# Kernel tuning notes

Measured on AMD Instinct MI355X. Metric: run time of the kernel, lower is better.

The kernel has to match this reference:

```python
import jax, jax.numpy as jnp
import numpy as np

IN_FEATURES, OUT_FEATURES, KERNEL_DIMS = 1024, 128, 8
BATCH = 256


def setup_inputs() -> dict:
    key = jax.random.key(0)
    kx, kT = jax.random.split(key)
    x = jax.random.normal(kx, (BATCH, IN_FEATURES), dtype=jnp.float32)
    T = jax.random.normal(kT, (IN_FEATURES, OUT_FEATURES, KERNEL_DIMS), dtype=jnp.float32)
    return {"x": x, "T": T}


def reference(x, T):
    B = x.shape[0]
    in_f, out_f, kd = T.shape
    # M: (B, out_features, kernel_dims)
    M = (x @ T.reshape(in_f, out_f * kd)).reshape(B, out_f, kd)
    # pairwise L1 distance over kernel dims: (B, B, out_features)
    diffs = jnp.abs(M[None, :, :, :] - M[:, None, :, :]).sum(axis=3)
    # similarity features: sum over other samples, subtract self-term (exp(0)=1)
    c = jnp.exp(-diffs).sum(axis=1) - 1.0  # (B, out_features)
    return jnp.concatenate([x, c], axis=1)
```

## Files before the change

kernel.cpp:

```cpp
#include <hip/hip_runtime.h>
#include <stdint.h>

#define BATCH 256
#define INF   1024
#define OUTF  128
#define KD    8
#define NN    1024
#define OROW  1152

#define TSLP  1040
#define MLS   12
#define CHSH  16384
#define NBUF  4

typedef __attribute__((ext_vector_type(8))) short short8;
typedef __attribute__((ext_vector_type(4))) float f32x4;

__device__ __forceinline__ unsigned short f2bf(float f) {
    union { float f; uint32_t u; } v; v.f = f;
    uint32_t r = v.u + 0x7FFFu + ((v.u >> 16) & 1u);
    return (unsigned short)(r >> 16);
}

__global__ __launch_bounds__(256) void prep_kernel(
    const float* __restrict__ x, const float* __restrict__ T,
    float* __restrict__ out, unsigned short* __restrict__ xbf,
    unsigned short* __restrict__ Tt)
{
    __shared__ unsigned short lds[64 * 65];
    int bid = blockIdx.x;
    int t = threadIdx.x;
    if (bid < 256) {
        int i0 = (bid >> 4) << 6;
        int n0 = (bid & 15) << 6;
        int tx = t & 63, ty = t >> 6;
        for (int r = ty; r < 64; r += 4) {
            float v = T[(size_t)(i0 + r) * NN + n0 + tx];
            lds[tx * 65 + r] = f2bf(v);
        }
        __syncthreads();
        #pragma unroll
        for (int p = 0; p < 8; ++p) {
            int q = p * 512 + t * 2;
            int n = q >> 6, i = q & 63;
            uint32_t u = (uint32_t)lds[n * 65 + i] | ((uint32_t)lds[n * 65 + i + 1] << 16);
            *(uint32_t*)(Tt + (size_t)(n0 + n) * INF + i0 + i) = u;
        }
    } else {
        int bx = bid - 256;
        #pragma unroll
        for (int p = 0; p < 4; ++p) {
            int a = bx * 4 + p;
            int j = t * 4;
            float4 v = *(const float4*)(x + (size_t)a * INF + j);
            *(float4*)(out + (size_t)a * OROW + j) = v;
            uint2 u;
            u.x = (uint32_t)f2bf(v.x) | ((uint32_t)f2bf(v.y) << 16);
            u.y = (uint32_t)f2bf(v.z) | ((uint32_t)f2bf(v.w) << 16);
            *(uint2*)(xbf + (size_t)a * INF + j) = u;
        }
    }
}

__device__ __forceinline__ void stage_xb(
    const unsigned short* __restrict__ xbf, unsigned short* lbuf,
    int c, int wave, int lane)
{
    const int rin = lane >> 3;
    const int seg = lane & 7;
    #pragma unroll
    for (int p = 0; p < 4; ++p) {
        const int i = wave * 4 + p;
        const unsigned short* src = xbf + (size_t)(i * 8 + rin) * INF
                                        + c * 64 + ((seg ^ rin) << 3);
        unsigned short* dst = lbuf + i * 512;
        __builtin_amdgcn_global_load_lds(
            (const __attribute__((address_space(1))) unsigned int*)src,
            (__attribute__((address_space(3))) unsigned int*)dst, 16, 0, 0);
    }
}

#define GEMM_STEP(c, VM) do {                                                 \
    const uint32_t bb = xlsBase + (uint32_t)(((c) & 3) << 15);                \
    const uint32_t tb = tslBase + (uint32_t)((c) << 7);                       \
    short8 A00, A01, A10, A11, B0, B1;                                        \
    asm volatile(                                                             \
        "s_waitcnt vmcnt(" #VM ")\n\t"                                        \
        "ds_read_b128 %0, %6\n\t"                                             \
        "ds_read_b128 %1, %7\n\t"                                             \
        "ds_read_b128 %2, %8\n\t"                                             \
        "ds_read_b128 %3, %9\n\t"                                             \
        "ds_read_b128 %4, %10\n\t"                                            \
        "ds_read_b128 %5, %11\n\t"                                            \
        "s_waitcnt lgkmcnt(0)"                                                \
        : "=v"(A00), "=v"(A01), "=v"(A10), "=v"(A11), "=v"(B0), "=v"(B1)      \
        : "v"(bb + oA00), "v"(bb + oA01), "v"(bb + oA10), "v"(bb + oA11),     \
          "v"(tb + oB0), "v"(tb + oB1)                                        \
        : "memory");                                                          \
    acc0 = __builtin_amdgcn_mfma_f32_16x16x32_bf16(A00, B0, acc0, 0, 0, 0);   \
    acc0 = __builtin_amdgcn_mfma_f32_16x16x32_bf16(A01, B1, acc0, 0, 0, 0);   \
    acc1 = __builtin_amdgcn_mfma_f32_16x16x32_bf16(A10, B0, acc1, 0, 0, 0);   \
    acc1 = __builtin_amdgcn_mfma_f32_16x16x32_bf16(A11, B1, acc1, 0, 0, 0);   \
} while (0)

__global__ __launch_bounds__(512, 1) void fused_kernel(
    const unsigned short* __restrict__ xbf, const unsigned short* __restrict__ Tt,
    float* __restrict__ out)
{
    __shared__ __align__(16) unsigned short xls[NBUF * CHSH];
    __shared__ __align__(16) union {
        unsigned short Tsl[KD * TSLP];
        float red[512];
    } u;
    __shared__ __align__(16) float Mloc[256 * MLS];

    const int o = blockIdx.x >> 1;
    const int half = blockIdx.x & 1;
    const int t = threadIdx.x;
    const int wave = t >> 6, lane = t & 63;

    #pragma unroll
    for (int p = 0; p < 2; ++p) {
        const unsigned short* src = Tt + (size_t)(o * 8 + wave) * INF + p * 512 + lane * 8;
        unsigned short* dst = u.Tsl + wave * TSLP + p * 512;
        __builtin_amdgcn_global_load_lds(
            (const __attribute__((address_space(1))) unsigned int*)src,
            (__attribute__((address_space(3))) unsigned int*)dst, 16, 0, 0);
    }
    stage_xb(xbf, xls + 0 * CHSH, 0, wave, lane);
    stage_xb(xbf, xls + 1 * CHSH, 1, wave, lane);
    stage_xb(xbf, xls + 2 * CHSH, 2, wave, lane);
    __syncthreads();

    const int rc = lane & 15, quad = lane >> 4, r7 = rc & 7;
    const int abase = wave * 32;
    f32x4 acc0 = {0.f, 0.f, 0.f, 0.f}, acc1 = {0.f, 0.f, 0.f, 0.f};

    const uint32_t xlsBase = (uint32_t)(uintptr_t)(&xls[0]);
    const uint32_t tslBase = (uint32_t)(uintptr_t)(&u.Tsl[0]);
    const uint32_t rowA = (uint32_t)((abase + rc) * 128);
    const uint32_t oA00 = rowA + (uint32_t)(((0 * 4 + quad) ^ r7) << 4);
    const uint32_t oA01 = rowA + (uint32_t)(((1 * 4 + quad) ^ r7) << 4);
    const uint32_t oA10 = oA00 + 2048, oA11 = oA01 + 2048;
    const uint32_t oB0 = (uint32_t)(r7 * 2080 + quad * 16);
    const uint32_t oB1 = oB0 + 64;

    for (int c = 0; c < 13; ++c) {
        stage_xb(xbf, xls + ((c + 3) & 3) * CHSH, c + 3, wave, lane);
        GEMM_STEP(c, 12);
    }
    GEMM_STEP(13, 8);
    GEMM_STEP(14, 4);
    GEMM_STEP(15, 0);

    if (rc < 8) {
        #pragma unroll
        for (int r = 0; r < 4; ++r) {
            Mloc[(abase + quad * 4 + r) * MLS + rc]      = acc0[r];
            Mloc[(abase + 16 + quad * 4 + r) * MLS + rc] = acc1[r];
        }
    }
    __syncthreads();

    const int ar = t & 127;
    const int bq = t >> 7;
    const int a = half * 128 + ar;
    f32x4 m0 = *(const f32x4*)(Mloc + a * MLS);
    f32x4 m1 = *(const f32x4*)(Mloc + a * MLS + 4);
    float ssum = 0.f;
    #pragma unroll 4
    for (int j = 0; j < 64; ++j) {
        const float* qp = Mloc + (bq * 64 + j) * MLS;
        f32x4 q0 = *(const f32x4*)(qp);
        f32x4 q1 = *(const f32x4*)(qp + 4);
        float d = fabsf(m0[0] - q0[0]) + fabsf(m0[1] - q0[1])
                + fabsf(m0[2] - q0[2]) + fabsf(m0[3] - q0[3])
                + fabsf(m1[0] - q1[0]) + fabsf(m1[1] - q1[1])
                + fabsf(m1[2] - q1[2]) + fabsf(m1[3] - q1[3]);
        ssum += __expf(-d);
    }
    u.red[t] = ssum;
    __syncthreads();
    if (t < 128) {
        float s = u.red[t] + u.red[t + 128] + u.red[t + 256] + u.red[t + 384];
        out[(size_t)(half * 128 + t) * OROW + INF + o] = s - 1.0f;
    }
}

extern "C" void kernel_launch(void* const* d_in, const int* in_sizes, int n_in,
                              void* d_out, int out_size, void* d_ws, size_t ws_size,
                              hipStream_t stream) {
    const float* x = (const float*)d_in[0];
    const float* T = (const float*)d_in[1];
    float* out = (float*)d_out;
    unsigned short* xbf = (unsigned short*)d_ws;
    unsigned short* Tt  = (unsigned short*)((char*)d_ws + 524288);

    prep_kernel<<<320, 256, 0, stream>>>(x, T, out, xbf, Tt);
    fused_kernel<<<256, 512, 0, stream>>>(xbf, Tt, out);
}
```

Baseline: 70.82 us.

## Switch GEMM operands from bf16 to fp8 MFMA with deeper LDS pipeline

Converts x and T to fp8 (e4m3) in the prep kernel instead of bf16 and uses the fp8 16x16x32 MFMA with 64-bit LDS reads. This halves workspace traffic and LDS footprint per chunk, and the freed space is used for an 8-deep staging pipeline with 7 chunks prefetched. The cost is a large precision drop: fp8 has about a 3-bit mantissa, and the values of M feed exp(-L1 distance) across 8 dims summed over 1024 inputs. That risks exceeding tolerance.

Measured after the change: 72.79 us. 1.03x slower.

```diff
diff --git a/kernel.cpp b/kernel.cpp
--- a/kernel.cpp
+++ b/kernel.cpp
@@ -8,26 +8,19 @@
 #define NN    1024
 #define OROW  1152
 
-#define TSLP  1040
 #define MLS   12
-#define CHSH  16384
-#define NBUF  4
+#define CHB   16384
+#define NBUF  8
+#define TP8   1056
 
-typedef __attribute__((ext_vector_type(8))) short short8;
 typedef __attribute__((ext_vector_type(4))) float f32x4;
-
-__device__ __forceinline__ unsigned short f2bf(float f) {
-    union { float f; uint32_t u; } v; v.f = f;
-    uint32_t r = v.u + 0x7FFFu + ((v.u >> 16) & 1u);
-    return (unsigned short)(r >> 16);
-}
 
 __global__ __launch_bounds__(256) void prep_kernel(
     const float* __restrict__ x, const float* __restrict__ T,
-    float* __restrict__ out, unsigned short* __restrict__ xbf,
-    unsigned short* __restrict__ Tt)
+    float* __restrict__ out, unsigned char* __restrict__ x8,
+    unsigned char* __restrict__ Tt8)
 {
-    __shared__ unsigned short lds[64 * 65];
+    __shared__ unsigned char lds8[64 * 68];
     int bid = blockIdx.x;
     int t = threadIdx.x;
     if (bid < 256) {
@@ -36,15 +29,16 @@
         int tx = t & 63, ty = t >> 6;
         for (int r = ty; r < 64; r += 4) {
             float v = T[(size_t)(i0 + r) * NN + n0 + tx];
-            lds[tx * 65 + r] = f2bf(v);
+            lds8[tx * 68 + r] =
+                (unsigned char)(__builtin_amdgcn_cvt_pk_fp8_f32(v, v, 0, false) & 0xff);
         }
         __syncthreads();
         #pragma unroll
-        for (int p = 0; p < 8; ++p) {
-            int q = p * 512 + t * 2;
+        for (int p = 0; p < 4; ++p) {
+            int q = p * 1024 + t * 4;
             int n = q >> 6, i = q & 63;
-            uint32_t u = (uint32_t)lds[n * 65 + i] | ((uint32_t)lds[n * 65 + i + 1] << 16);
-            *(uint32_t*)(Tt + (size_t)(n0 + n) * INF + i0 + i) = u;
+            uint32_t w = *(const uint32_t*)(lds8 + n * 68 + i);
+            *(uint32_t*)(Tt8 + (size_t)(n0 + n) * INF + i0 + i) = w;
         }
     } else {
         int bx = bid - 256;
@@ -54,26 +48,25 @@
             int j = t * 4;
             float4 v = *(const float4*)(x + (size_t)a * INF + j);
             *(float4*)(out + (size_t)a * OROW + j) = v;
-            uint2 u;
-            u.x = (uint32_t)f2bf(v.x) | ((uint32_t)f2bf(v.y) << 16);
-            u.y = (uint32_t)f2bf(v.z) | ((uint32_t)f2bf(v.w) << 16);
-            *(uint2*)(xbf + (size_t)a * INF + j) = u;
+            uint32_t w = (uint32_t)__builtin_amdgcn_cvt_pk_fp8_f32(v.x, v.y, 0, false);
+            w = (uint32_t)__builtin_amdgcn_cvt_pk_fp8_f32(v.z, v.w, (int)w, true);
+            *(uint32_t*)(x8 + (size_t)a * INF + j) = w;
         }
     }
 }
 
-__device__ __forceinline__ void stage_xb(
-    const unsigned short* __restrict__ xbf, unsigned short* lbuf,
+__device__ __forceinline__ void stage_x8(
+    const unsigned char* __restrict__ x8, unsigned char* lbuf,
     int c, int wave, int lane)
 {
-    const int rin = lane >> 3;
-    const int seg = lane & 7;
+    const int r16 = lane >> 2;
+    const int slot = lane & 3;
     #pragma unroll
-    for (int p = 0; p < 4; ++p) {
-        const int i = wave * 4 + p;
-        const unsigned short* src = xbf + (size_t)(i * 8 + rin) * INF
-                                        + c * 64 + ((seg ^ rin) << 3);
-        unsigned short* dst = lbuf + i * 512;
+    for (int p = 0; p < 2; ++p) {
+        const int i = wave * 2 + p;
+        const unsigned char* src = x8 + (size_t)(i * 16 + r16) * INF
+                                       + c * 64 + ((slot ^ (r16 & 3)) << 4);
+        unsigned char* dst = lbuf + i * 1024;
         __builtin_amdgcn_global_load_lds(
             (const __attribute__((address_space(1))) unsigned int*)src,
             (__attribute__((address_space(3))) unsigned int*)dst, 16, 0, 0);
@@ -81,35 +74,35 @@
 }
 
 #define GEMM_STEP(c, VM) do {                                                 \
-    const uint32_t bb = xlsBase + (uint32_t)(((c) & 3) << 15);                \
-    const uint32_t tb = tslBase + (uint32_t)((c) << 7);                       \
-    short8 A00, A01, A10, A11, B0, B1;                                        \
+    const uint32_t bb = xlsBase + (uint32_t)(((c) & 7) * CHB);                \
+    const uint32_t tb = tslBase + oB + (uint32_t)((c) << 6);                  \
+    long long A00, A01, A10, A11, B0, B1;                                     \
     asm volatile(                                                             \
         "s_waitcnt vmcnt(" #VM ")\n\t"                                        \
-        "ds_read_b128 %0, %6\n\t"                                             \
-        "ds_read_b128 %1, %7\n\t"                                             \
-        "ds_read_b128 %2, %8\n\t"                                             \
-        "ds_read_b128 %3, %9\n\t"                                             \
-        "ds_read_b128 %4, %10\n\t"                                            \
-        "ds_read_b128 %5, %11\n\t"                                            \
+        "ds_read_b64 %0, %6\n\t"                                              \
+        "ds_read_b64 %1, %7\n\t"                                              \
+        "ds_read_b64 %2, %8\n\t"                                              \
+        "ds_read_b64 %3, %9\n\t"                                              \
+        "ds_read_b64 %4, %10\n\t"                                             \
+        "ds_read_b64 %5, %11\n\t"                                             \
         "s_waitcnt lgkmcnt(0)"                                                \
         : "=v"(A00), "=v"(A01), "=v"(A10), "=v"(A11), "=v"(B0), "=v"(B1)      \
-        : "v"(bb + oA00), "v"(bb + oA01), "v"(bb + oA10), "v"(bb + oA11),     \
-          "v"(tb + oB0), "v"(tb + oB1)                                        \
+        : "v"(bb + aA00), "v"(bb + aA01), "v"(bb + aA00 + 1024),              \
+          "v"(bb + aA01 + 1024), "v"(tb), "v"(tb + 32)                        \
         : "memory");                                                          \
-    acc0 = __builtin_amdgcn_mfma_f32_16x16x32_bf16(A00, B0, acc0, 0, 0, 0);   \
-    acc0 = __builtin_amdgcn_mfma_f32_16x16x32_bf16(A01, B1, acc0, 0, 0, 0);   \
-    acc1 = __builtin_amdgcn_mfma_f32_16x16x32_bf16(A10, B0, acc1, 0, 0, 0);   \
-    acc1 = __builtin_amdgcn_mfma_f32_16x16x32_bf16(A11, B1, acc1, 0, 0, 0);   \
+    acc0 = __builtin_amdgcn_mfma_f32_16x16x32_fp8_fp8(A00, B0, acc0, 0, 0, 0);\
+    acc0 = __builtin_amdgcn_mfma_f32_16x16x32_fp8_fp8(A01, B1, acc0, 0, 0, 0);\
+    acc1 = __builtin_amdgcn_mfma_f32_16x16x32_fp8_fp8(A10, B0, acc1, 0, 0, 0);\
+    acc1 = __builtin_amdgcn_mfma_f32_16x16x32_fp8_fp8(A11, B1, acc1, 0, 0, 0);\
 } while (0)
 
 __global__ __launch_bounds__(512, 1) void fused_kernel(
-    const unsigned short* __restrict__ xbf, const unsigned short* __restrict__ Tt,
+    const unsigned char* __restrict__ x8, const unsigned char* __restrict__ Tt8,
     float* __restrict__ out)
 {
-    __shared__ __align__(16) unsigned short xls[NBUF * CHSH];
+    __shared__ __align__(16) unsigned char xls[NBUF * CHB];
     __shared__ __align__(16) union {
-        unsigned short Tsl[KD * TSLP];
+        unsigned char Tsl[8 * TP8];
         float red[512];
     } u;
     __shared__ __align__(16) float Mloc[256 * MLS];
@@ -119,38 +112,41 @@
     const int t = threadIdx.x;
     const int wave = t >> 6, lane = t & 63;
 
-    #pragma unroll
-    for (int p = 0; p < 2; ++p) {
-        const unsigned short* src = Tt + (size_t)(o * 8 + wave) * INF + p * 512 + lane * 8;
-        unsigned short* dst = u.Tsl + wave * TSLP + p * 512;
+    {
+        const unsigned char* src = Tt8 + (size_t)(o * 8 + wave) * INF + lane * 16;
+        unsigned char* dst = u.Tsl + wave * TP8;
         __builtin_amdgcn_global_load_lds(
             (const __attribute__((address_space(1))) unsigned int*)src,
             (__attribute__((address_space(3))) unsigned int*)dst, 16, 0, 0);
     }
-    stage_xb(xbf, xls + 0 * CHSH, 0, wave, lane);
-    stage_xb(xbf, xls + 1 * CHSH, 1, wave, lane);
-    stage_xb(xbf, xls + 2 * CHSH, 2, wave, lane);
+    #pragma unroll
+    for (int c = 0; c < 7; ++c)
+        stage_x8(x8, xls + c * CHB, c, wave, lane);
     __syncthreads();
 
-    const int rc = lane & 15, quad = lane >> 4, r7 = rc & 7;
+    const int rc = lane & 15, quad = lane >> 4;
     const int abase = wave * 32;
     f32x4 acc0 = {0.f, 0.f, 0.f, 0.f}, acc1 = {0.f, 0.f, 0.f, 0.f};
 
     const uint32_t xlsBase = (uint32_t)(uintptr_t)(&xls[0]);
     const uint32_t tslBase = (uint32_t)(uintptr_t)(&u.Tsl[0]);
-    const uint32_t rowA = (uint32_t)((abase + rc) * 128);
-    const uint32_t oA00 = rowA + (uint32_t)(((0 * 4 + quad) ^ r7) << 4);
-    const uint32_t oA01 = rowA + (uint32_t)(((1 * 4 + quad) ^ r7) << 4);
-    const uint32_t oA10 = oA00 + 2048, oA11 = oA01 + 2048;
-    const uint32_t oB0 = (uint32_t)(r7 * 2080 + quad * 16);
-    const uint32_t oB1 = oB0 + 64;
+    const uint32_t rowOff = (uint32_t)((abase + rc) * 64);
+    const uint32_t aA00 = rowOff
+        + (uint32_t)(((((quad >> 1)) ^ (rc & 3)) << 4) + (quad & 1) * 8);
+    const uint32_t aA01 = rowOff
+        + (uint32_t)((((2 + (quad >> 1)) ^ (rc & 3)) << 4) + (quad & 1) * 8);
+    const uint32_t oB = (uint32_t)((rc & 7) * TP8 + quad * 8);
 
-    for (int c = 0; c < 13; ++c) {
-        stage_xb(xbf, xls + ((c + 3) & 3) * CHSH, c + 3, wave, lane);
-        GEMM_STEP(c, 12);
+    for (int c = 0; c < 9; ++c) {
+        stage_x8(x8, xls + ((c + 7) & 7) * CHB, c + 7, wave, lane);
+        GEMM_STEP(c, 14);
     }
-    GEMM_STEP(13, 8);
-    GEMM_STEP(14, 4);
+    GEMM_STEP(9, 12);
+    GEMM_STEP(10, 10);
+    GEMM_STEP(11, 8);
+    GEMM_STEP(12, 6);
+    GEMM_STEP(13, 4);
+    GEMM_STEP(14, 2);
     GEMM_STEP(15, 0);
 
     if (rc < 8) {
@@ -193,9 +189,9 @@
     const float* x = (const float*)d_in[0];
     const float* T = (const float*)d_in[1];
     float* out = (float*)d_out;
-    unsigned short* xbf = (unsigned short*)d_ws;
-    unsigned short* Tt  = (unsigned short*)((char*)d_ws + 524288);
+    unsigned char* x8  = (unsigned char*)d_ws;
+    unsigned char* Tt8 = (unsigned char*)d_ws + 262144;
 
-    prep_kernel<<<320, 256, 0, stream>>>(x, T, out, xbf, Tt);
-    fused_kernel<<<256, 512, 0, stream>>>(xbf, Tt, out);
+    prep_kernel<<<320, 256, 0, stream>>>(x, T, out, x8, Tt8);
+    fused_kernel<<<256, 512, 0, stream>>>(x8, Tt8, out);
 }
```

## Double fused kernel to 1024 threads, one 16-row MFMA tile per wave

Applied to the files above, without the earlier changes.

Moves the fused GEMM+similarity kernel from 512 to 1024 threads per block. Each wave now owns a single 16-row M tile and splits the K chunk across two accumulators that are summed at the end. Staging loads per wave, wait counts and the pairwise loop length are halved, and the final reduction sums 8 partials instead of 4. The aim is more waves per CU to hide latency, at the price of a larger block and more reduction and sync overhead.

New measurement: 70.74 us. Within noise of the previous version (-0.1%).

```diff
diff --git a/kernel.cpp b/kernel.cpp
--- a/kernel.cpp
+++ b/kernel.cpp
@@ -69,8 +69,8 @@
     const int rin = lane >> 3;
     const int seg = lane & 7;
     #pragma unroll
-    for (int p = 0; p < 4; ++p) {
-        const int i = wave * 4 + p;
+    for (int p = 0; p < 2; ++p) {
+        const int i = wave * 2 + p;
         const unsigned short* src = xbf + (size_t)(i * 8 + rin) * INF
                                         + c * 64 + ((seg ^ rin) << 3);
         unsigned short* dst = lbuf + i * 512;
@@ -83,34 +83,29 @@
 #define GEMM_STEP(c, VM) do {                                                 \
     const uint32_t bb = xlsBase + (uint32_t)(((c) & 3) << 15);                \
     const uint32_t tb = tslBase + (uint32_t)((c) << 7);                       \
-    short8 A00, A01, A10, A11, B0, B1;                                        \
+    short8 A0, A1, B0, B1;                                                    \
     asm volatile(                                                             \
         "s_waitcnt vmcnt(" #VM ")\n\t"                                        \
-        "ds_read_b128 %0, %6\n\t"                                             \
-        "ds_read_b128 %1, %7\n\t"                                             \
-        "ds_read_b128 %2, %8\n\t"                                             \
-        "ds_read_b128 %3, %9\n\t"                                             \
-        "ds_read_b128 %4, %10\n\t"                                            \
-        "ds_read_b128 %5, %11\n\t"                                            \
+        "ds_read_b128 %0, %4\n\t"                                             \
+        "ds_read_b128 %1, %5\n\t"                                             \
+        "ds_read_b128 %2, %6\n\t"                                             \
+        "ds_read_b128 %3, %7\n\t"                                             \
         "s_waitcnt lgkmcnt(0)"                                                \
-        : "=v"(A00), "=v"(A01), "=v"(A10), "=v"(A11), "=v"(B0), "=v"(B1)      \
-        : "v"(bb + oA00), "v"(bb + oA01), "v"(bb + oA10), "v"(bb + oA11),     \
-          "v"(tb + oB0), "v"(tb + oB1)                                        \
+        : "=v"(A0), "=v"(A1), "=v"(B0), "=v"(B1)                              \
+        : "v"(bb + oA0), "v"(bb + oA1), "v"(tb + oB0), "v"(tb + oB1)          \
         : "memory");                                                          \
-    acc0 = __builtin_amdgcn_mfma_f32_16x16x32_bf16(A00, B0, acc0, 0, 0, 0);   \
-    acc0 = __builtin_amdgcn_mfma_f32_16x16x32_bf16(A01, B1, acc0, 0, 0, 0);   \
-    acc1 = __builtin_amdgcn_mfma_f32_16x16x32_bf16(A10, B0, acc1, 0, 0, 0);   \
-    acc1 = __builtin_amdgcn_mfma_f32_16x16x32_bf16(A11, B1, acc1, 0, 0, 0);   \
+    acc0 = __builtin_amdgcn_mfma_f32_16x16x32_bf16(A0, B0, acc0, 0, 0, 0);    \
+    acc1 = __builtin_amdgcn_mfma_f32_16x16x32_bf16(A1, B1, acc1, 0, 0, 0);    \
 } while (0)
 
-__global__ __launch_bounds__(512, 1) void fused_kernel(
+__global__ __launch_bounds__(1024, 1) void fused_kernel(
     const unsigned short* __restrict__ xbf, const unsigned short* __restrict__ Tt,
     float* __restrict__ out)
 {
     __shared__ __align__(16) unsigned short xls[NBUF * CHSH];
     __shared__ __align__(16) union {
         unsigned short Tsl[KD * TSLP];
-        float red[512];
+        float red[1024];
     } u;
     __shared__ __align__(16) float Mloc[256 * MLS];
 
@@ -119,13 +114,15 @@
     const int t = threadIdx.x;
     const int wave = t >> 6, lane = t & 63;
 
-    #pragma unroll
-    for (int p = 0; p < 2; ++p) {
-        const unsigned short* src = Tt + (size_t)(o * 8 + wave) * INF + p * 512 + lane * 8;
-        unsigned short* dst = u.Tsl + wave * TSLP + p * 512;
-        __builtin_amdgcn_global_load_lds(
-            (const __attribute__((address_space(1))) unsigned int*)src,
-            (__attribute__((address_space(3))) unsigned int*)dst, 16, 0, 0);
+    if (wave < 8) {
+        #pragma unroll
+        for (int p = 0; p < 2; ++p) {
+            const unsigned short* src = Tt + (size_t)(o * 8 + wave) * INF + p * 512 + lane * 8;
+            unsigned short* dst = u.Tsl + wave * TSLP + p * 512;
+            __builtin_amdgcn_global_load_lds(
+                (const __attribute__((address_space(1))) unsigned int*)src,
+                (__attribute__((address_space(3))) unsigned int*)dst, 16, 0, 0);
+        }
     }
     stage_xb(xbf, xls + 0 * CHSH, 0, wave, lane);
     stage_xb(xbf, xls + 1 * CHSH, 1, wave, lane);
@@ -133,32 +130,28 @@
     __syncthreads();
 
     const int rc = lane & 15, quad = lane >> 4, r7 = rc & 7;
-    const int abase = wave * 32;
     f32x4 acc0 = {0.f, 0.f, 0.f, 0.f}, acc1 = {0.f, 0.f, 0.f, 0.f};
 
     const uint32_t xlsBase = (uint32_t)(uintptr_t)(&xls[0]);
     const uint32_t tslBase = (uint32_t)(uintptr_t)(&u.Tsl[0]);
-    const uint32_t rowA = (uint32_t)((abase + rc) * 128);
-    const uint32_t oA00 = rowA + (uint32_t)(((0 * 4 + quad) ^ r7) << 4);
-    const uint32_t oA01 = rowA + (uint32_t)(((1 * 4 + quad) ^ r7) << 4);
-    const uint32_t oA10 = oA00 + 2048, oA11 = oA01 + 2048;
+    const uint32_t rowA = (uint32_t)((wave * 16 + rc) * 128);
+    const uint32_t oA0 = rowA + (uint32_t)(((0 * 4 + quad) ^ r7) << 4);
+    const uint32_t oA1 = rowA + (uint32_t)(((1 * 4 + quad) ^ r7) << 4);
     const uint32_t oB0 = (uint32_t)(r7 * 2080 + quad * 16);
     const uint32_t oB1 = oB0 + 64;
 
     for (int c = 0; c < 13; ++c) {
         stage_xb(xbf, xls + ((c + 3) & 3) * CHSH, c + 3, wave, lane);
-        GEMM_STEP(c, 12);
+        GEMM_STEP(c, 6);
     }
-    GEMM_STEP(13, 8);
-    GEMM_STEP(14, 4);
+    GEMM_STEP(13, 4);
+    GEMM_STEP(14, 2);
     GEMM_STEP(15, 0);
 
     if (rc < 8) {
         #pragma unroll
-        for (int r = 0; r < 4; ++r) {
-            Mloc[(abase + quad * 4 + r) * MLS + rc]      = acc0[r];
-            Mloc[(abase + 16 + quad * 4 + r) * MLS + rc] = acc1[r];
-        }
+        for (int r = 0; r < 4; ++r)
+            Mloc[(wave * 16 + quad * 4 + r) * MLS + rc] = acc0[r] + acc1[r];
     }
     __syncthreads();
 
@@ -169,8 +162,8 @@
     f32x4 m1 = *(const f32x4*)(Mloc + a * MLS + 4);
     float ssum = 0.f;
     #pragma unroll 4
-    for (int j = 0; j < 64; ++j) {
-        const float* qp = Mloc + (bq * 64 + j) * MLS;
+    for (int j = 0; j < 32; ++j) {
+        const float* qp = Mloc + (bq * 32 + j) * MLS;
         f32x4 q0 = *(const f32x4*)(qp);
         f32x4 q1 = *(const f32x4*)(qp + 4);
         float d = fabsf(m0[0] - q0[0]) + fabsf(m0[1] - q0[1])
@@ -182,7 +175,9 @@
     u.red[t] = ssum;
     __syncthreads();
     if (t < 128) {
-        float s = u.red[t] + u.red[t + 128] + u.red[t + 256] + u.red[t + 384];
+        float s = 0.f;
+        #pragma unroll
+        for (int q = 0; q < 8; ++q) s += u.red[t + q * 128];
         out[(size_t)(half * 128 + t) * OROW + INF + o] = s - 1.0f;
     }
 }
@@ -197,5 +192,5 @@
     unsigned short* Tt  = (unsigned short*)((char*)d_ws + 524288);
 
     prep_kernel<<<320, 256, 0, stream>>>(x, T, out, xbf, Tt);
-    fused_kernel<<<256, 512, 0, stream>>>(xbf, Tt, out);
+    fused_kernel<<<256, 1024, 0, stream>>>(xbf, Tt, out);
 }
```

## Fuse T transpose and bf16 conversion into the main kernel's LDS staging

Applied to the files above, without the earlier changes.

The separate transpose/convert pass over T (256 blocks writing a transposed bf16 copy to workspace) is removed from the prep kernel. Each fused block now reads its 8-column float slice of T straight from global memory, converts it to bf16 and scatters it transposed into LDS. This saves one full write and re-read of T through global memory and shrinks the prep launch. The cost is strided float4 reads of T (32 bytes per row) and scalar 2-byte LDS stores, done synchronously before the GEMM starts. Each T slice is read by both blocks that share the same output column.

Result: slower. 74.29 us (+4.9%).

```diff
diff --git a/kernel.cpp b/kernel.cpp
--- a/kernel.cpp
+++ b/kernel.cpp
@@ -23,42 +23,20 @@
 }
 
 __global__ __launch_bounds__(256) void prep_kernel(
-    const float* __restrict__ x, const float* __restrict__ T,
-    float* __restrict__ out, unsigned short* __restrict__ xbf,
-    unsigned short* __restrict__ Tt)
+    const float* __restrict__ x, float* __restrict__ out,
+    unsigned short* __restrict__ xbf)
 {
-    __shared__ unsigned short lds[64 * 65];
-    int bid = blockIdx.x;
-    int t = threadIdx.x;
-    if (bid < 256) {
-        int i0 = (bid >> 4) << 6;
-        int n0 = (bid & 15) << 6;
-        int tx = t & 63, ty = t >> 6;
-        for (int r = ty; r < 64; r += 4) {
-            float v = T[(size_t)(i0 + r) * NN + n0 + tx];
-            lds[tx * 65 + r] = f2bf(v);
-        }
-        __syncthreads();
-        #pragma unroll
-        for (int p = 0; p < 8; ++p) {
-            int q = p * 512 + t * 2;
-            int n = q >> 6, i = q & 63;
-            uint32_t u = (uint32_t)lds[n * 65 + i] | ((uint32_t)lds[n * 65 + i + 1] << 16);
-            *(uint32_t*)(Tt + (size_t)(n0 + n) * INF + i0 + i) = u;
-        }
-    } else {
-        int bx = bid - 256;
-        #pragma unroll
-        for (int p = 0; p < 4; ++p) {
-            int a = bx * 4 + p;
-            int j = t * 4;
-            float4 v = *(const float4*)(x + (size_t)a * INF + j);
-            *(float4*)(out + (size_t)a * OROW + j) = v;
-            uint2 u;
-            u.x = (uint32_t)f2bf(v.x) | ((uint32_t)f2bf(v.y) << 16);
-            u.y = (uint32_t)f2bf(v.z) | ((uint32_t)f2bf(v.w) << 16);
-            *(uint2*)(xbf + (size_t)a * INF + j) = u;
-        }
+    int bx = blockIdx.x, t = threadIdx.x;
+    #pragma unroll
+    for (int p = 0; p < 4; ++p) {
+        int a = bx * 4 + p;
+        int j = t * 4;
+        float4 v = *(const float4*)(x + (size_t)a * INF + j);
+        *(float4*)(out + (size_t)a * OROW + j) = v;
+        uint2 u;
+        u.x = (uint32_t)f2bf(v.x) | ((uint32_t)f2bf(v.y) << 16);
+        u.y = (uint32_t)f2bf(v.z) | ((uint32_t)f2bf(v.w) << 16);
+        *(uint2*)(xbf + (size_t)a * INF + j) = u;
     }
 }
 
@@ -104,7 +82,7 @@
 } while (0)
 
 __global__ __launch_bounds__(512, 1) void fused_kernel(
-    const unsigned short* __restrict__ xbf, const unsigned short* __restrict__ Tt,
+    const unsigned short* __restrict__ xbf, const float* __restrict__ T,
     float* __restrict__ out)
 {
     __shared__ __align__(16) unsigned short xls[NBUF * CHSH];
@@ -119,17 +97,20 @@
     const int t = threadIdx.x;
     const int wave = t >> 6, lane = t & 63;
 
-    #pragma unroll
-    for (int p = 0; p < 2; ++p) {
-        const unsigned short* src = Tt + (size_t)(o * 8 + wave) * INF + p * 512 + lane * 8;
-        unsigned short* dst = u.Tsl + wave * TSLP + p * 512;
-        __builtin_amdgcn_global_load_lds(
-            (const __attribute__((address_space(1))) unsigned int*)src,
-            (__attribute__((address_space(3))) unsigned int*)dst, 16, 0, 0);
-    }
     stage_xb(xbf, xls + 0 * CHSH, 0, wave, lane);
     stage_xb(xbf, xls + 1 * CHSH, 1, wave, lane);
     stage_xb(xbf, xls + 2 * CHSH, 2, wave, lane);
+
+    #pragma unroll
+    for (int it = 0; it < 4; ++it) {
+        int i = it * 512 + t;
+        int k = i >> 1, h = (i & 1) * 4;
+        float4 v = *(const float4*)(T + (size_t)k * NN + o * KD + h);
+        u.Tsl[(h + 0) * TSLP + k] = f2bf(v.x);
+        u.Tsl[(h + 1) * TSLP + k] = f2bf(v.y);
+        u.Tsl[(h + 2) * TSLP + k] = f2bf(v.z);
+        u.Tsl[(h + 3) * TSLP + k] = f2bf(v.w);
+    }
     __syncthreads();
 
     const int rc = lane & 15, quad = lane >> 4, r7 = rc & 7;
@@ -194,8 +175,7 @@
     const float* T = (const float*)d_in[1];
     float* out = (float*)d_out;
     unsigned short* xbf = (unsigned short*)d_ws;
-    unsigned short* Tt  = (unsigned short*)((char*)d_ws + 524288);
 
-    prep_kernel<<<320, 256, 0, stream>>>(x, T, out, xbf, Tt);
-    fused_kernel<<<256, 512, 0, stream>>>(xbf, Tt, out);
+    prep_kernel<<<64, 256, 0, stream>>>(x, out, xbf);
+    fused_kernel<<<256, 512, 0, stream>>>(xbf, T, out);
 }
```
